# Kernel tuning notes

Measured on AMD Instinct MI355X. Metric: run time of the kernel, lower is better.

Reference implementation:

```python
import jax, jax.numpy as jnp
import numpy as np

D_MODEL = 1024
NUM_HEADS = 16
DEPTH = D_MODEL // NUM_HEADS


def setup_inputs() -> dict:
    key = jax.random.key(0)
    ks = jax.random.split(key, 11)
    B, S = 4, 2048
    scale = 1.0 / np.sqrt(D_MODEL)
    inp = {
        "query": jax.random.normal(ks[0], (B, S, D_MODEL), jnp.float32),
        "key": jax.random.normal(ks[1], (B, S, D_MODEL), jnp.float32),
        "value": jax.random.normal(ks[2], (B, S, D_MODEL), jnp.float32),
        # Linear params (torch nn.Linear: y = x @ W.T + b); store W as [out, in]
        "wq_w": jax.random.normal(ks[3], (D_MODEL, D_MODEL), jnp.float32) * scale,
        "wq_b": jnp.zeros((D_MODEL,), jnp.float32),
        "wk_w": jax.random.normal(ks[4], (D_MODEL, D_MODEL), jnp.float32) * scale,
        "wk_b": jnp.zeros((D_MODEL,), jnp.float32),
        "wv_w": jax.random.normal(ks[5], (D_MODEL, D_MODEL), jnp.float32) * scale,
        "wv_b": jnp.zeros((D_MODEL,), jnp.float32),
        "dense_w": jax.random.normal(ks[6], (D_MODEL, D_MODEL), jnp.float32) * scale,
        "dense_b": jnp.zeros((D_MODEL,), jnp.float32),
    }
    return inp


def _split_heads(x, B):
    # [B, S, D] -> [B, H, S, depth]
    return x.reshape(B, -1, NUM_HEADS, DEPTH).transpose(0, 2, 1, 3)


def reference(query, key, value, wq_w, wq_b, wk_w, wk_b, wv_w, wv_b, dense_w, dense_b):
    B = query.shape[0]
    q = _split_heads(query @ wq_w.T + wq_b, B)   # [B,H,Sq,depth]
    k = _split_heads(key @ wk_w.T + wk_b, B)     # [B,H,Sk,depth]
    v = _split_heads(value @ wv_w.T + wv_b, B)   # [B,H,Sk,depth]
    scores = jnp.einsum("bhqd,bhkd->bhqk", q, k) / jnp.sqrt(jnp.float32(DEPTH)).astype(q.dtype)
    attn = jax.nn.softmax(scores, axis=-1)
    out = jnp.einsum("bhqk,bhkd->bhqd", attn, v)  # [B,H,Sq,depth]
    out = out.transpose(0, 2, 1, 3).reshape(B, -1, D_MODEL)
    return out @ dense_w.T + dense_b
```

## Files before the change

kernel.cpp:

```cpp
#include <hip/hip_runtime.h>
#include <hip/hip_bf16.h>
#include <stdint.h>


#define SEQ    2048
#define DEPTH  64
#define HEADS  16
#define NMODEL 1024
#define MROWS  8192

typedef __bf16 bf16x8 __attribute__((ext_vector_type(8)));
typedef float  f32x4  __attribute__((ext_vector_type(4)));

__device__ __forceinline__ unsigned short f32_bf16(float f) {
    union { float f; unsigned int u; } c; c.f = f;
    unsigned int u = c.u + 0x7FFFu + ((c.u >> 16) & 1u);
    return (unsigned short)(u >> 16);
}

__device__ __forceinline__ void gload16(const unsigned short* g, unsigned short* l) {
    __builtin_amdgcn_global_load_lds(
        (const __attribute__((address_space(1))) unsigned int*)g,
        (__attribute__((address_space(3))) unsigned int*)l, 16, 0, 0);
}

__global__ __launch_bounds__(256) void cvt3_kernel(
    const float* __restrict__ a, const float* __restrict__ b, const float* __restrict__ c,
    unsigned short* __restrict__ oa, unsigned short* __restrict__ ob,
    unsigned short* __restrict__ oc, int n4)
{
    const float* in; unsigned short* out;
    if (blockIdx.y == 0) { in = a; out = oa; }
    else if (blockIdx.y == 1) { in = b; out = ob; }
    else { in = c; out = oc; }
    int i = blockIdx.x * 256 + threadIdx.x;
    if (i < n4) {
        float4 f = ((const float4*)in)[i];
        ushort4 o;
        o.x = f32_bf16(f.x); o.y = f32_bf16(f.y);
        o.z = f32_bf16(f.z); o.w = f32_bf16(f.w);
        ((ushort4*)out)[i] = o;
    }
}

__global__ __launch_bounds__(256) void cvt4_kernel(
    const float* __restrict__ a, const float* __restrict__ b,
    const float* __restrict__ c, const float* __restrict__ d,
    unsigned short* __restrict__ oa, unsigned short* __restrict__ ob,
    unsigned short* __restrict__ oc, unsigned short* __restrict__ od, int n4)
{
    const float* in; unsigned short* out;
    if (blockIdx.y == 0) { in = a; out = oa; }
    else if (blockIdx.y == 1) { in = b; out = ob; }
    else if (blockIdx.y == 2) { in = c; out = oc; }
    else { in = d; out = od; }
    int i = blockIdx.x * 256 + threadIdx.x;
    if (i < n4) {
        float4 f = ((const float4*)in)[i];
        ushort4 o;
        o.x = f32_bf16(f.x); o.y = f32_bf16(f.y);
        o.z = f32_bf16(f.z); o.w = f32_bf16(f.w);
        ((ushort4*)out)[i] = o;
    }
}

__device__ __forceinline__ void gemm128_core(
    const unsigned short* __restrict__ A, const unsigned short* __restrict__ W,
    const float* __restrict__ bias, void* __restrict__ outp,
    int mode, float scale, int m0, int n0,
    unsigned short* Alds, unsigned short* Blds)
{
    const int tid  = threadIdx.x;
    const int wave = tid >> 6, lane = tid & 63;
    const int l15  = lane & 15, quad = lane >> 4;
    const int wm   = wave & 1,  wn   = wave >> 1;
    const int swz  = l15 & 7;
    const int K    = 1024;

    f32x4 acc[4][4] = {};

    const int lrow = lane >> 3;
    const int fcol = ((lane & 7) ^ lrow) << 3;
    const unsigned short* Ab[4];
    const unsigned short* Bb[4];
    #pragma unroll
    for (int c = 0; c < 4; ++c) {
        const int seg = 4 * wave + c;
        Ab[c] = A + (size_t)(m0 + seg * 8 + lrow) * K + fcol;
        Bb[c] = W + (size_t)(n0 + seg * 8 + lrow) * K + fcol;
    }

    for (int k0 = 0; k0 < K; k0 += 64) {
        #pragma unroll
        for (int c = 0; c < 4; ++c) {
            gload16(Ab[c] + k0, &Alds[(4 * wave + c) * 512]);
            gload16(Bb[c] + k0, &Blds[(4 * wave + c) * 512]);
        }
        __syncthreads();

        #pragma unroll
        for (int kc = 0; kc < 2; ++kc) {
            bf16x8 a[4], b[4];
            const int pg = (((kc * 4 + quad) ^ swz) << 3);
            #pragma unroll
            for (int i = 0; i < 4; ++i)
                a[i] = *(const bf16x8*)&Alds[(wm * 64 + i * 16 + l15) * 64 + pg];
            #pragma unroll
            for (int j = 0; j < 4; ++j)
                b[j] = *(const bf16x8*)&Blds[(wn * 64 + j * 16 + l15) * 64 + pg];
            #pragma unroll
            for (int i = 0; i < 4; ++i)
                #pragma unroll
                for (int j = 0; j < 4; ++j)
                    acc[i][j] = __builtin_amdgcn_mfma_f32_16x16x32_bf16(a[i], b[j], acc[i][j], 0, 0, 0);
        }
        __syncthreads();
    }

    #pragma unroll
    for (int i = 0; i < 4; ++i) {
        #pragma unroll
        for (int j = 0; j < 4; ++j) {
            const int col = n0 + wn * 64 + j * 16 + l15;
            const int row_b = m0 + wm * 64 + i * 16 + quad * 4;
            if (mode == 2) {
                #pragma unroll
                for (int r = 0; r < 4; ++r) {
                    const int row = row_b + r;
                    ((unsigned short*)outp)[(size_t)row * MROWS + col] =
                        f32_bf16(acc[i][j][r] + bias[row]);
                }
            } else if (mode == 0) {
                const float bv = bias[col];
                #pragma unroll
                for (int r = 0; r < 4; ++r)
                    ((float*)outp)[(size_t)(row_b + r) * NMODEL + col] = acc[i][j][r] + bv;
            } else {
                const float bv = bias[col];
                const int h_ = col >> 6, d_ = col & 63;
                #pragma unroll
                for (int r = 0; r < 4; ++r) {
                    const int row = row_b + r;
                    const int b_ = row >> 11, s_ = row & 2047;
                    ((unsigned short*)outp)[(((size_t)(b_ * HEADS + h_) * SEQ + s_) << 6) + d_] =
                        f32_bf16((acc[i][j][r] + bv) * scale);
                }
            }
        }
    }
}

__global__ __launch_bounds__(256, 3) void gemm_qkv(
    const unsigned short* __restrict__ qb,  const unsigned short* __restrict__ wqb,
    const float* __restrict__ bq, unsigned short* __restrict__ Qp,
    const unsigned short* __restrict__ kb,  const unsigned short* __restrict__ wkb,
    const float* __restrict__ bk, unsigned short* __restrict__ Kpj,
    const unsigned short* __restrict__ wvb, const unsigned short* __restrict__ vb,
    const float* __restrict__ bv, unsigned short* __restrict__ Vtg,
    float qscale)
{
    __shared__ unsigned short Alds[128 * 64];
    __shared__ unsigned short Blds[128 * 64];
    const int bid = blockIdx.x, z = blockIdx.y;
    if (z == 0) {
        gemm128_core(qb, wqb, bq, Qp, 1, qscale, (bid >> 3) * 128, (bid & 7) * 128, Alds, Blds);
    } else if (z == 1) {
        gemm128_core(kb, wkb, bk, Kpj, 1, 1.0f, (bid >> 3) * 128, (bid & 7) * 128, Alds, Blds);
    } else {
        gemm128_core(wvb, vb, bv, Vtg, 2, 1.0f, (bid & 7) * 128, (bid >> 3) * 128, Alds, Blds);
    }
}

__global__ __launch_bounds__(256, 3) void gemm_dense(
    const unsigned short* __restrict__ A, const unsigned short* __restrict__ W,
    const float* __restrict__ bias, float* __restrict__ out)
{
    __shared__ unsigned short Alds[128 * 64];
    __shared__ unsigned short Blds[128 * 64];
    const int bid = blockIdx.x;
    gemm128_core(A, W, bias, out, 0, 1.0f, (bid >> 3) * 128, (bid & 7) * 128, Alds, Blds);
}

__global__ __launch_bounds__(256, 4) void attn_fwd(
    const unsigned short* __restrict__ Qp,
    const unsigned short* __restrict__ Kp,
    const unsigned short* __restrict__ Vtg,
    unsigned short* __restrict__ Op)
{
    __shared__ unsigned short Klds[64 * 64];
    __shared__ unsigned short Vlds[64 * 64];
    __shared__ unsigned short Pt[4 * 32 * 64];
    const int tid  = threadIdx.x;
    const int wave = tid >> 6, lane = tid & 63;
    const int l15  = lane & 15, quad = lane >> 4;
    const int swz  = l15 & 7;
    const int bh   = blockIdx.y;
    const int b_   = bh >> 4, h_ = bh & 15;
    const int q0   = blockIdx.x * 128;

    const unsigned short* Qb = Qp + (size_t)bh * SEQ * DEPTH;
    const unsigned short* Kb = Kp + (size_t)bh * SEQ * DEPTH;
    const unsigned short* Vb = Vtg + (size_t)h_ * DEPTH * MROWS + (size_t)b_ * SEQ;

    const int srow = (wave << 3) + (lane >> 3);
    const int scg  = (lane & 7) ^ ((lane >> 3) & 7);
    unsigned short* KldsW = &Klds[wave * 512];
    unsigned short* VldsW = &Vlds[wave * 512];
    unsigned short* PtW   = &Pt[wave * 2048];

    bf16x8 qf[2][2];
    #pragma unroll
    for (int i = 0; i < 2; ++i)
        #pragma unroll
        for (int kc = 0; kc < 2; ++kc)
            qf[i][kc] = *(const bf16x8*)(Qb + (size_t)(q0 + wave * 32 + i * 16 + l15) * DEPTH
                                         + kc * 32 + quad * 8);

    f32x4 Ot[2][4] = {};
    float lsum[2] = {0.f, 0.f};

    for (int kt = 0; kt < SEQ / 64; ++kt) {
        const int kb0 = kt * 64;
        gload16(Kb + (size_t)(kb0 + srow) * DEPTH + scg * 8,      KldsW);
        gload16(Kb + (size_t)(kb0 + srow + 32) * DEPTH + scg * 8, KldsW + 2048);
        gload16(Vb + (size_t)srow * MROWS + kb0 + scg * 8,        VldsW);
        gload16(Vb + (size_t)(srow + 32) * MROWS + kb0 + scg * 8, VldsW + 2048);
        __syncthreads();

        f32x4 St[2][4];
        #pragma unroll
        for (int i = 0; i < 2; ++i)
            #pragma unroll
            for (int jj = 0; jj < 4; ++jj)
                St[i][jj] = f32x4{};
        #pragma unroll
        for (int jj = 0; jj < 4; ++jj) {
            bf16x8 k0 = *(const bf16x8*)&Klds[(jj * 16 + l15) * 64 + (((quad    ) ^ swz) << 3)];
            bf16x8 k1 = *(const bf16x8*)&Klds[(jj * 16 + l15) * 64 + (((4 + quad) ^ swz) << 3)];
            #pragma unroll
            for (int i = 0; i < 2; ++i) {
                St[i][jj] = __builtin_amdgcn_mfma_f32_16x16x32_bf16(k0, qf[i][0], St[i][jj], 0, 0, 0);
                St[i][jj] = __builtin_amdgcn_mfma_f32_16x16x32_bf16(k1, qf[i][1], St[i][jj], 0, 0, 0);
            }
        }

        #pragma unroll
        for (int i = 0; i < 2; ++i) {
            #pragma unroll
            for (int jj = 0; jj < 4; ++jj) {
                float p0 = __builtin_amdgcn_exp2f(St[i][jj][0]);
                float p1 = __builtin_amdgcn_exp2f(St[i][jj][1]);
                float p2 = __builtin_amdgcn_exp2f(St[i][jj][2]);
                float p3 = __builtin_amdgcn_exp2f(St[i][jj][3]);
                lsum[i] += (p0 + p1) + (p2 + p3);
                __hip_bfloat162 pa = __float22bfloat162_rn(make_float2(p0, p1));
                __hip_bfloat162 pb = __float22bfloat162_rn(make_float2(p2, p3));
                uint2 pw = { *(unsigned int*)&pa, *(unsigned int*)&pb };
                *(uint2*)&PtW[(i * 16 + l15) * 64 +
                              (((2 * jj + (quad >> 1)) ^ swz) << 3) + (quad & 1) * 4] = pw;
            }
        }

        #pragma unroll
        for (int kc = 0; kc < 2; ++kc) {
            const int pg = (((kc * 4 + quad) ^ swz) << 3);
            bf16x8 vf[4];
            #pragma unroll
            for (int dd = 0; dd < 4; ++dd)
                vf[dd] = *(const bf16x8*)&Vlds[(dd * 16 + l15) * 64 + pg];
            #pragma unroll
            for (int i = 0; i < 2; ++i) {
                bf16x8 pf = *(const bf16x8*)&PtW[(i * 16 + l15) * 64 + pg];
                #pragma unroll
                for (int dd = 0; dd < 4; ++dd)
                    Ot[i][dd] = __builtin_amdgcn_mfma_f32_16x16x32_bf16(vf[dd], pf, Ot[i][dd], 0, 0, 0);
            }
        }
        __syncthreads();
    }

    #pragma unroll
    for (int i = 0; i < 2; ++i) {
        lsum[i] += __shfl_xor(lsum[i], 16, 64);
        lsum[i] += __shfl_xor(lsum[i], 32, 64);
    }

    #pragma unroll
    for (int i = 0; i < 2; ++i) {
        const float inv = 1.0f / lsum[i];
        const int row = b_ * SEQ + q0 + wave * 32 + i * 16 + l15;
        #pragma unroll
        for (int dd = 0; dd < 4; ++dd) {
            ushort4 ov;
            ov.x = f32_bf16(Ot[i][dd][0] * inv);
            ov.y = f32_bf16(Ot[i][dd][1] * inv);
            ov.z = f32_bf16(Ot[i][dd][2] * inv);
            ov.w = f32_bf16(Ot[i][dd][3] * inv);
            const int col = h_ * 64 + dd * 16 + quad * 4;
            *(ushort4*)&Op[(size_t)row * NMODEL + col] = ov;
        }
    }
}

extern "C" void kernel_launch(void* const* d_in, const int* in_sizes, int n_in,
                              void* d_out, int out_size, void* d_ws, size_t ws_size,
                              hipStream_t stream) {
    const float* q  = (const float*)d_in[0];
    const float* k  = (const float*)d_in[1];
    const float* v  = (const float*)d_in[2];
    const float* wq = (const float*)d_in[3];
    const float* bq = (const float*)d_in[4];
    const float* wk = (const float*)d_in[5];
    const float* bk = (const float*)d_in[6];
    const float* wv = (const float*)d_in[7];
    const float* bv = (const float*)d_in[8];
    const float* wd = (const float*)d_in[9];
    const float* bd = (const float*)d_in[10];

    char* ws = (char*)d_ws;
    size_t off = 0;
    auto alloc = [&](size_t bytes) { char* p = ws + off; off += bytes; return p; };
    const size_t ACT = (size_t)MROWS * NMODEL * 2;
    const size_t WGT = (size_t)NMODEL * NMODEL * 2;

    unsigned short* qb   = (unsigned short*)alloc(ACT);
    unsigned short* kb   = (unsigned short*)alloc(ACT);
    unsigned short* vb   = (unsigned short*)alloc(ACT);
    unsigned short* wqb  = (unsigned short*)alloc(WGT);
    unsigned short* wkb  = (unsigned short*)alloc(WGT);
    unsigned short* wvb  = (unsigned short*)alloc(WGT);
    unsigned short* wdb  = (unsigned short*)alloc(WGT);
    unsigned short* Qp   = (unsigned short*)alloc(ACT);
    unsigned short* Kpj  = (unsigned short*)alloc(ACT);
    unsigned short* Vtg  = (unsigned short*)alloc(ACT);
    unsigned short* attn = (unsigned short*)alloc(ACT);

    const int nAct4 = MROWS * NMODEL / 4;
    const int nWgt4 = NMODEL * NMODEL / 4;
    cvt3_kernel<<<dim3(nAct4 / 256, 3), 256, 0, stream>>>(q, k, v, qb, kb, vb, nAct4);
    cvt4_kernel<<<dim3(nWgt4 / 256, 4), 256, 0, stream>>>(wq, wk, wv, wd,
                                                          wqb, wkb, wvb, wdb, nWgt4);

    const float SC = 0.18033688011112042f;
    gemm_qkv<<<dim3(512, 3), 256, 0, stream>>>(qb, wqb, bq, Qp,
                                               kb, wkb, bk, Kpj,
                                               wvb, vb, bv, Vtg, SC);

    attn_fwd<<<dim3(SEQ / 128, 64), 256, 0, stream>>>(Qp, Kpj, Vtg, attn);

    gemm_dense<<<512, 256, 0, stream>>>(attn, wdb, bd, (float*)d_out);
}
```

Before: 342.9 us.

## Give each attention wave 64 query rows and compute row sums with MFMA

The attention block is cut to 2 waves of 128 threads, each owning 64 query rows instead of 32. This doubles the reuse of every K/V tile loaded into LDS per wave and halves the block-level K/V load cost per query. The QK^T score, exp and P store are fused per 16-row slice, and the softmax denominator is now accumulated by an extra MFMA against a ones vector instead of scalar adds plus shuffles. The trade-off is higher register pressure (Ot[4][4] plus lacc), fewer waves per block for latency hiding, and 4 extra MFMAs per tile.

```diff
diff --git a/kernel.cpp b/kernel.cpp
--- a/kernel.cpp
+++ b/kernel.cpp
@@ -181,7 +181,7 @@
     gemm128_core(A, W, bias, out, 0, 1.0f, (bid >> 3) * 128, (bid & 7) * 128, Alds, Blds);
 }
 
-__global__ __launch_bounds__(256, 4) void attn_fwd(
+__global__ __launch_bounds__(128, 3) void attn_fwd(
     const unsigned short* __restrict__ Qp,
     const unsigned short* __restrict__ Kp,
     const unsigned short* __restrict__ Vtg,
@@ -189,70 +189,63 @@
 {
     __shared__ unsigned short Klds[64 * 64];
     __shared__ unsigned short Vlds[64 * 64];
-    __shared__ unsigned short Pt[4 * 32 * 64];
+    __shared__ unsigned short Pt[2][64 * 64];
     const int tid  = threadIdx.x;
     const int wave = tid >> 6, lane = tid & 63;
     const int l15  = lane & 15, quad = lane >> 4;
     const int swz  = l15 & 7;
     const int bh   = blockIdx.y;
     const int b_   = bh >> 4, h_ = bh & 15;
-    const int q0   = blockIdx.x * 128;
+    const int q0   = blockIdx.x * 128 + wave * 64;
 
     const unsigned short* Qb = Qp + (size_t)bh * SEQ * DEPTH;
     const unsigned short* Kb = Kp + (size_t)bh * SEQ * DEPTH;
     const unsigned short* Vb = Vtg + (size_t)h_ * DEPTH * MROWS + (size_t)b_ * SEQ;
 
-    const int srow = (wave << 3) + (lane >> 3);
-    const int scg  = (lane & 7) ^ ((lane >> 3) & 7);
-    unsigned short* KldsW = &Klds[wave * 512];
-    unsigned short* VldsW = &Vlds[wave * 512];
-    unsigned short* PtW   = &Pt[wave * 2048];
-
-    bf16x8 qf[2][2];
+    const int lrow = lane >> 3;
+    const int scg  = (lane & 7) ^ lrow;
+    unsigned short* PtW = Pt[wave];
+
+    bf16x8 qf[4][2];
     #pragma unroll
-    for (int i = 0; i < 2; ++i)
+    for (int i = 0; i < 4; ++i)
         #pragma unroll
         for (int kc = 0; kc < 2; ++kc)
-            qf[i][kc] = *(const bf16x8*)(Qb + (size_t)(q0 + wave * 32 + i * 16 + l15) * DEPTH
+            qf[i][kc] = *(const bf16x8*)(Qb + (size_t)(q0 + i * 16 + l15) * DEPTH
                                          + kc * 32 + quad * 8);
 
-    f32x4 Ot[2][4] = {};
-    float lsum[2] = {0.f, 0.f};
+    f32x4 Ot[4][4] = {};
+    f32x4 lacc[4] = {};
+    const __bf16 one = (__bf16)1.0f;
+    const bf16x8 onesf = {one, one, one, one, one, one, one, one};
 
     for (int kt = 0; kt < SEQ / 64; ++kt) {
         const int kb0 = kt * 64;
-        gload16(Kb + (size_t)(kb0 + srow) * DEPTH + scg * 8,      KldsW);
-        gload16(Kb + (size_t)(kb0 + srow + 32) * DEPTH + scg * 8, KldsW + 2048);
-        gload16(Vb + (size_t)srow * MROWS + kb0 + scg * 8,        VldsW);
-        gload16(Vb + (size_t)(srow + 32) * MROWS + kb0 + scg * 8, VldsW + 2048);
+        #pragma unroll
+        for (int c = 0; c < 4; ++c) {
+            const int rc = c * 16 + wave * 8;
+            gload16(Kb + (size_t)(kb0 + rc + lrow) * DEPTH + scg * 8, &Klds[rc * 64]);
+        }
+        #pragma unroll
+        for (int c = 0; c < 4; ++c) {
+            const int rc = c * 16 + wave * 8;
+            gload16(Vb + (size_t)(rc + lrow) * MROWS + kb0 + scg * 8, &Vlds[rc * 64]);
+        }
         __syncthreads();
 
-        f32x4 St[2][4];
-        #pragma unroll
-        for (int i = 0; i < 2; ++i)
-            #pragma unroll
-            for (int jj = 0; jj < 4; ++jj)
-                St[i][jj] = f32x4{};
         #pragma unroll
         for (int jj = 0; jj < 4; ++jj) {
-            bf16x8 k0 = *(const bf16x8*)&Klds[(jj * 16 + l15) * 64 + (((quad    ) ^ swz) << 3)];
-            bf16x8 k1 = *(const bf16x8*)&Klds[(jj * 16 + l15) * 64 + (((4 + quad) ^ swz) << 3)];
-            #pragma unroll
-            for (int i = 0; i < 2; ++i) {
-                St[i][jj] = __builtin_amdgcn_mfma_f32_16x16x32_bf16(k0, qf[i][0], St[i][jj], 0, 0, 0);
-                St[i][jj] = __builtin_amdgcn_mfma_f32_16x16x32_bf16(k1, qf[i][1], St[i][jj], 0, 0, 0);
-            }
-        }
-
-        #pragma unroll
-        for (int i = 0; i < 2; ++i) {
-            #pragma unroll
-            for (int jj = 0; jj < 4; ++jj) {
-                float p0 = __builtin_amdgcn_exp2f(St[i][jj][0]);
-                float p1 = __builtin_amdgcn_exp2f(St[i][jj][1]);
-                float p2 = __builtin_amdgcn_exp2f(St[i][jj][2]);
-                float p3 = __builtin_amdgcn_exp2f(St[i][jj][3]);
-                lsum[i] += (p0 + p1) + (p2 + p3);
+            bf16x8 kf0 = *(const bf16x8*)&Klds[(jj * 16 + l15) * 64 + (((quad    ) ^ swz) << 3)];
+            bf16x8 kf1 = *(const bf16x8*)&Klds[(jj * 16 + l15) * 64 + (((4 + quad) ^ swz) << 3)];
+            #pragma unroll
+            for (int i = 0; i < 4; ++i) {
+                f32x4 s = {};
+                s = __builtin_amdgcn_mfma_f32_16x16x32_bf16(kf0, qf[i][0], s, 0, 0, 0);
+                s = __builtin_amdgcn_mfma_f32_16x16x32_bf16(kf1, qf[i][1], s, 0, 0, 0);
+                float p0 = __builtin_amdgcn_exp2f(s[0]);
+                float p1 = __builtin_amdgcn_exp2f(s[1]);
+                float p2 = __builtin_amdgcn_exp2f(s[2]);
+                float p3 = __builtin_amdgcn_exp2f(s[3]);
                 __hip_bfloat162 pa = __float22bfloat162_rn(make_float2(p0, p1));
                 __hip_bfloat162 pb = __float22bfloat162_rn(make_float2(p2, p3));
                 uint2 pw = { *(unsigned int*)&pa, *(unsigned int*)&pb };
@@ -269,8 +262,9 @@
             for (int dd = 0; dd < 4; ++dd)
                 vf[dd] = *(const bf16x8*)&Vlds[(dd * 16 + l15) * 64 + pg];
             #pragma unroll
-            for (int i = 0; i < 2; ++i) {
+            for (int i = 0; i < 4; ++i) {
                 bf16x8 pf = *(const bf16x8*)&PtW[(i * 16 + l15) * 64 + pg];
+                lacc[i] = __builtin_amdgcn_mfma_f32_16x16x32_bf16(onesf, pf, lacc[i], 0, 0, 0);
                 #pragma unroll
                 for (int dd = 0; dd < 4; ++dd)
                     Ot[i][dd] = __builtin_amdgcn_mfma_f32_16x16x32_bf16(vf[dd], pf, Ot[i][dd], 0, 0, 0);
@@ -280,15 +274,9 @@
     }
 
     #pragma unroll
-    for (int i = 0; i < 2; ++i) {
-        lsum[i] += __shfl_xor(lsum[i], 16, 64);
-        lsum[i] += __shfl_xor(lsum[i], 32, 64);
-    }
-
-    #pragma unroll
-    for (int i = 0; i < 2; ++i) {
-        const float inv = 1.0f / lsum[i];
-        const int row = b_ * SEQ + q0 + wave * 32 + i * 16 + l15;
+    for (int i = 0; i < 4; ++i) {
+        const float inv = 1.0f / lacc[i][0];
+        const int row = b_ * SEQ + q0 + i * 16 + l15;
         #pragma unroll
         for (int dd = 0; dd < 4; ++dd) {
             ushort4 ov;
@@ -346,7 +334,7 @@
                                                kb, wkb, bk, Kpj,
                                                wvb, vb, bv, Vtg, SC);
 
-    attn_fwd<<<dim3(SEQ / 128, 64), 256, 0, stream>>>(Qp, Kpj, Vtg, attn);
+    attn_fwd<<<dim3(SEQ / 128, 64), 128, 0, stream>>>(Qp, Kpj, Vtg, attn);
 
     gemm_dense<<<512, 256, 0, stream>>>(attn, wdb, bd, (float*)d_out);
 }
```

Result: slower. 407.4 us (+18.8%).
